# Kernel optimization log

Hardware: AMD Instinct MI355X
Metric: run time of the kernel (lower is better)

## Reference

```python
import jax, jax.numpy as jnp
import numpy as np

SCALES = (1, 2, 4, 8, 16, 32, 64, 128)
BETA = 0.25   # args.commit_beta
B, C, T = 64, 512, 128
Q, V = 8, 1024
DEPTH, K = 2, 3


def setup_inputs() -> dict:
    key = jax.random.key(0)
    k1, k2, k3, k4 = jax.random.split(key, 4)
    z = jax.random.normal(k1, (B, C, T), dtype=jnp.float32)
    codebooks = jax.random.normal(k2, (Q, V, C), dtype=jnp.float32)
    # small init so stacked ReLU convs stay numerically sane (fan_in = C*K)
    phi_w = jax.random.normal(k3, (Q, DEPTH, C, C, K), dtype=jnp.float32) * (1.0 / np.sqrt(C * K))
    phi_b = jax.random.normal(k4, (Q, DEPTH, C), dtype=jnp.float32) * 0.01
    return {"z": z, "codebooks": codebooks, "phi_w": phi_w, "phi_b": phi_b}


def _conv1d(x, w, b):
    # x: (B,C,T), w: (C_out,C_in,K), 'same' padding (K//2)
    y = jax.lax.conv_general_dilated(x, w, window_strides=(1,), padding=[(K // 2, K // 2)],
                                     dimension_numbers=('NCH', 'OIH', 'NCH'))
    return y + b[None, :, None]


def _phi(x, w_q, b_q):
    # Phi: DEPTH x (Conv1d + ReLU)
    for d in range(DEPTH):
        x = jax.nn.relu(_conv1d(x, w_q[d], b_q[d]))
    return x


def _quantize(xd, cb):
    # xd: (B,C,s) -> nearest codebook entry per timestep. cb: (V,C)
    s = xd.shape[-1]
    flat = xd.transpose(0, 2, 1).reshape(-1, C)                      # (B*s, C)
    d = (jnp.sum(flat * flat, axis=1, keepdims=True)
         - 2.0 * flat @ cb.T + jnp.sum(cb * cb, axis=1))            # (B*s, V)
    idx = jnp.argmin(d, axis=1)                                      # (B*s,)
    emb = cb[idx].reshape(B, s, C).transpose(0, 2, 1)                # (B,C,s)
    # straight-through (EMA codebook: no grad to codebook)
    quant = xd + jax.lax.stop_gradient(emb - xd)
    return quant, idx.reshape(B, s)


def reference(z, codebooks, phi_w, phi_b):
    z = z.astype(jnp.float32)
    z_ng = jax.lax.stop_gradient(z)
    z_q = z_ng
    z_hat = jnp.zeros_like(z_q)
    losses, usages, perps, all_idx = [], [], [], []
    for q, s in enumerate(SCALES):
        # area downsample == window mean (T divisible by s)
        xd = z_q.reshape(B, C, s, T // s).mean(axis=-1)              # (B,C,s)
        quant, idx = _quantize(xd, codebooks[q])
        up = quant if s == T else jax.image.resize(quant, (B, C, T), method='linear')
        z_hat_q = _phi(up, phi_w[q], phi_b[q])
        z_hat = z_hat + z_hat_q
        z_q = z_q - z_hat_q
        counts = jnp.zeros((V,), jnp.float32).at[idx.ravel()].add(1.0)
        usages.append(jnp.mean((counts > 0).astype(jnp.float32)) * 100.0)
        p = counts / (B * s)
        perps.append(jnp.exp(-jnp.sum(p * jnp.log(p + 1e-10))))
        losses.append(BETA * jnp.mean((jax.lax.stop_gradient(z_hat) - z) ** 2)
                      + jnp.mean((z_hat - z_ng) ** 2))
        all_idx.append(idx)
    nQ = float(len(SCALES))
    usage = sum(usages) / nQ
    loss = sum(losses) / nQ
    perp = sum(perps) / nQ
    z_hat_out = jax.lax.stop_gradient(z_hat) - z_ng + z              # straight-through output
    indices = jnp.concatenate([i for i in all_idx], axis=1)          # (B, sum(scales))
    return z_hat_out, usage, loss, perp, indices
```

## Files before the change

### kernel.cpp

```cpp
#include <hip/hip_runtime.h>
#include <math.h>

#define NB 64
#define NC 512
#define NT 128
#define NQ 8
#define NV 1024
#define NBIG 4194304
#define IDX_STRIDE 255

typedef _Float16 half_t;
typedef half_t f16x8 __attribute__((ext_vector_type(8)));
typedef float  f32x4 __attribute__((ext_vector_type(4)));

#define SC_MAIN 0.015625f
#define SC_MID  2.44140625e-4f

#define GLD16(g, l) __builtin_amdgcn_global_load_lds( \
    (const __attribute__((address_space(1))) unsigned int*)(g), \
    (__attribute__((address_space(3))) unsigned int*)(l), 16, 0, 0)

__device__ inline void split64(float v, half_t& h1, half_t& h2) {
    half_t a = (half_t)(v * 64.f);
    float r = v * 64.f - (float)a;
    h1 = a;
    h2 = (half_t)(r * 64.f);
}
__device__ inline void split1(float v, half_t& h1, half_t& h2) {
    half_t a = (half_t)v;
    float r = v - (float)a;
    h1 = a;
    h2 = (half_t)(r * 64.f);
}

__global__ void init_kernel(float* __restrict__ zhat, int* __restrict__ counts,
                            float* __restrict__ accums) {
    int i = blockIdx.x * 256 + threadIdx.x;
    const int stride = 2048 * 256;
    for (; i < NBIG; i += stride) {
        zhat[i] = 0.f;
        if (i < NQ * NV) counts[i] = 0;
        if (i < 16)      accums[i] = 0.f;
    }
}

__global__ void padzero_kernel(half_t* __restrict__ X1, half_t* __restrict__ X2) {
    int b = blockIdx.x;
    int row = blockIdx.y ? 129 : 0;
    int c = threadIdx.x;
    size_t off = ((size_t)b * 130 + row) * NC + c;
    X1[off] = (half_t)0.f; X2[off] = (half_t)0.f;
}

__global__ void cnorm_kernel(const float* __restrict__ cb, float* __restrict__ cnorm) {
    int wid  = (blockIdx.x * 256 + threadIdx.x) >> 6;
    int lane = threadIdx.x & 63;
    if (wid >= NQ * NV) return;
    const float* row = cb + (size_t)wid * NC;
    float s = 0.f;
    #pragma unroll
    for (int e = 0; e < NC / 64; ++e) { float v = row[lane + e * 64]; s = fmaf(v, v, s); }
    #pragma unroll
    for (int m = 32; m >= 1; m >>= 1) s += __shfl_xor(s, m, 64);
    if (lane == 0) cnorm[wid] = s;
}

__global__ void cbprep_kernel(const float* __restrict__ cb, half_t* __restrict__ CbT) {
    int idx = blockIdx.x * 256 + threadIdx.x;
    int e  = idx & 8191;
    int kt = (idx >> 13) & 7;
    int mt = (idx >> 16) & 7;
    int q  = idx >> 19;
    int m = e >> 6, kk = e & 63;
    int ci = kt * 64 + kk;
    int code = mt * 128 + m;
    float v = cb[((size_t)(q * NV + code)) * NC + ci];
    half_t h1, h2;
    split64(v, h1, h2);
    int off = ((m * 128 + kk * 2) ^ ((m & 7) << 4)) >> 1;
    size_t base = ((((size_t)q * 2 + 0) * 8 + mt) * 8 + kt) * 8192 + off;
    CbT[base] = h1;
    CbT[base + (size_t)8 * 8 * 8192] = h2;
}

__global__ __launch_bounds__(256) void downsample_split_kernel(
        const float* __restrict__ z, const float* __restrict__ zhat,
        half_t* __restrict__ Xd1, half_t* __restrict__ Xd2,
        int s, int log2s) {
    __shared__ float D[64 * 129];
    const int tid = threadIdx.x;
    const int b  = blockIdx.x;
    const int c0 = blockIdx.y << 6;
    const size_t gbase = ((size_t)(b * NC + c0)) * NT;
    #pragma unroll
    for (int i = 0; i < 8; ++i) {
        int idx4 = (i * 256 + tid) * 4;
        float4 zv = *(const float4*)(z    + gbase + idx4);
        float4 hv = *(const float4*)(zhat + gbase + idx4);
        int cc = idx4 >> 7, t = idx4 & 127;
        float* dp = D + cc * 129 + t;
        dp[0] = zv.x - hv.x; dp[1] = zv.y - hv.y; dp[2] = zv.z - hv.z; dp[3] = zv.w - hv.w;
    }
    __syncthreads();
    const int w = NT >> log2s;
    const float invw = 1.f / (float)w;
    for (int idx = tid; idx < (s << 6); idx += 256) {
        int cc = idx & 63;
        int j  = idx >> 6;
        const float* row = D + cc * 129 + j * w;
        float sum = 0.f;
        for (int i = 0; i < w; ++i) sum += row[i];
        float xd = sum * invw;
        half_t h1, h2;
        split1(xd, h1, h2);
        size_t o = ((size_t)(b * s + j)) * NC + c0 + cc;
        Xd1[o] = h1;
        Xd2[o] = h2;
    }
}

__global__ __launch_bounds__(256, 2) void quant_mfma_kernel(
        const half_t* __restrict__ CbTq,
        const half_t* __restrict__ Xd1, const half_t* __restrict__ Xd2,
        const float* __restrict__ cnorm,
        float* __restrict__ pval, int* __restrict__ pidx) {
    __shared__ half_t As1[8192];
    __shared__ half_t As2[8192];
    __shared__ half_t Bs1[4096];
    __shared__ half_t Bs2[4096];
    __shared__ float redv[2][2][2][16];
    __shared__ int   redi[2][2][2][16];
    const int tid = threadIdx.x;
    const int w = tid >> 6, l = tid & 63;
    const int wm = w >> 1, wn = w & 1;
    const int lane16 = l & 15, lhi = l >> 4;
    const int nblk = blockIdx.x, mt = blockIdx.y;
    const int r0 = nblk * 64;
    f32x4 accM[4][2] = {}, accm[4][2] = {};
    const half_t* C1b = CbTq + ((size_t)(0 * 8 + mt)) * (8 * 8192);
    const half_t* C2b = CbTq + ((size_t)(1 * 8 + mt)) * (8 * 8192);
    for (int kt = 0; kt < 8; ++kt) {
        const int ci0 = kt << 6;
        __syncthreads();
        const char* c1src = (const char*)(C1b + (size_t)kt * 8192);
        const char* c2src = (const char*)(C2b + (size_t)kt * 8192);
        #pragma unroll
        for (int i = 0; i < 4; ++i) {
            GLD16(c1src + (i * 256 + tid) * 16, (char*)As1 + i * 4096 + w * 1024);
            GLD16(c2src + (i * 256 + tid) * 16, (char*)As2 + i * 4096 + w * 1024);
        }
        #pragma unroll
        for (int i = 0; i < 2; ++i) {
            int c = i * 256 + tid;
            int n = c >> 3, sub = c & 7;
            size_t soff = ((size_t)(r0 + n)) * NC + ci0 + ((sub ^ (n & 7)) << 3);
            GLD16(Xd1 + soff, (char*)Bs1 + i * 4096 + w * 1024);
            GLD16(Xd2 + soff, (char*)Bs2 + i * 4096 + w * 1024);
        }
        __syncthreads();
        #pragma unroll
        for (int kstep = 0; kstep < 2; ++kstep) {
            const int kb = (kstep * 32 + lhi * 8) * 2;
            f16x8 a1[4], a2[4], b1[2], b2[2];
            #pragma unroll
            for (int im = 0; im < 4; ++im) {
                int m = wm * 64 + im * 16 + lane16;
                int off = (m * 128 + kb) ^ ((m & 7) << 4);
                a1[im] = *(const f16x8*)((const char*)As1 + off);
                a2[im] = *(const f16x8*)((const char*)As2 + off);
            }
            #pragma unroll
            for (int in = 0; in < 2; ++in) {
                int n = wn * 32 + in * 16 + lane16;
                int off = (n * 128 + kb) ^ ((n & 7) << 4);
                b1[in] = *(const f16x8*)((const char*)Bs1 + off);
                b2[in] = *(const f16x8*)((const char*)Bs2 + off);
            }
            #pragma unroll
            for (int im = 0; im < 4; ++im)
                #pragma unroll
                for (int in = 0; in < 2; ++in) {
                    accM[im][in] = __builtin_amdgcn_mfma_f32_16x16x32_f16(a1[im], b1[in], accM[im][in], 0, 0, 0);
                    accm[im][in] = __builtin_amdgcn_mfma_f32_16x16x32_f16(a1[im], b2[in], accm[im][in], 0, 0, 0);
                    accm[im][in] = __builtin_amdgcn_mfma_f32_16x16x32_f16(a2[im], b1[in], accm[im][in], 0, 0, 0);
                }
        }
    }
    float bv[2] = {1e30f, 1e30f};
    int   bi[2] = {0, 0};
    #pragma unroll
    for (int im = 0; im < 4; ++im) {
        int mb = mt * 128 + wm * 64 + im * 16 + lhi * 4;
        float4 cn = *(const float4*)(cnorm + mb);
        const float* cnp = (const float*)&cn;
        #pragma unroll
        for (int in = 0; in < 2; ++in) {
            #pragma unroll
            for (int r = 0; r < 4; ++r) {
                float d = cnp[r] - 2.f * (accM[im][in][r] * SC_MAIN + accm[im][in][r] * SC_MID);
                int code = mb + r;
                if (d < bv[in]) { bv[in] = d; bi[in] = code; }
            }
        }
    }
    #pragma unroll
    for (int m = 16; m <= 32; m <<= 1) {
        #pragma unroll
        for (int in = 0; in < 2; ++in) {
            float ov = __shfl_xor(bv[in], m, 64);
            int   oi = __shfl_xor(bi[in], m, 64);
            if (ov < bv[in] || (ov == bv[in] && oi < bi[in])) { bv[in] = ov; bi[in] = oi; }
        }
    }
    if (lhi == 0) {
        #pragma unroll
        for (int in = 0; in < 2; ++in) { redv[wm][wn][in][lane16] = bv[in]; redi[wm][wn][in][lane16] = bi[in]; }
    }
    __syncthreads();
    if (wm == 0 && lhi == 0) {
        #pragma unroll
        for (int in = 0; in < 2; ++in) {
            float v0 = redv[0][wn][in][lane16]; int i0 = redi[0][wn][in][lane16];
            float v1 = redv[1][wn][in][lane16]; int i1 = redi[1][wn][in][lane16];
            if (v1 < v0 || (v1 == v0 && i1 < i0)) { v0 = v1; i0 = i1; }
            int r = r0 + wn * 32 + in * 16 + lane16;
            pval[(size_t)r * 8 + mt] = v0;
            pidx[(size_t)r * 8 + mt] = i0;
        }
    }
}

__global__ void argmin_final_kernel(const float* __restrict__ pval, const int* __restrict__ pidx,
                                    int* __restrict__ idx_int, int* __restrict__ counts,
                                    float* __restrict__ out_idx, int R, int s, int log2s, int offq) {
    int r = blockIdx.x * 256 + threadIdx.x;
    if (r >= R) return;
    float bv = 1e30f; int bi = 0;
    #pragma unroll
    for (int k = 0; k < 8; ++k) {
        float v = pval[(size_t)r * 8 + k];
        int   i = pidx[(size_t)r * 8 + k];
        if (v < bv || (v == bv && i < bi)) { bv = v; bi = i; }
    }
    idx_int[r] = bi;
    atomicAdd(&counts[bi], 1);
    int b = r >> log2s, j = r & (s - 1);
    out_idx[(size_t)b * IDX_STRIDE + offq + j] = (float)bi;
}

__global__ void upsample_split_kernel(const float* __restrict__ cb, const int* __restrict__ idx_int,
                                      half_t* __restrict__ X1, half_t* __restrict__ X2, int s) {
    int b = blockIdx.x, tp = blockIdx.y, c = threadIdx.x;
    size_t off = ((size_t)b * 130 + tp) * NC + c;
    if (tp == 0 || tp == 129) { X1[off] = (half_t)0.f; X2[off] = (half_t)0.f; return; }
    int t = tp - 1;
    float in = (t + 0.5f) * ((float)s * (1.f / 128.f)) - 0.5f;
    float jf = floorf(in);
    float f = in - jf;
    int j0 = (int)jf;
    int i0 = min(max(j0, 0), s - 1);
    int i1 = min(max(j0 + 1, 0), s - 1);
    const int* ib = idx_int + b * s;
    float v0 = cb[(size_t)ib[i0] * NC + c];
    float v1 = cb[(size_t)ib[i1] * NC + c];
    float v = (1.f - f) * v0 + f * v1;
    half_t h1, h2;
    split1(v, h1, h2);
    X1[off] = h1; X2[off] = h2;
}

__global__ void wprep_kernel(const float* __restrict__ W ,
                             half_t* __restrict__ Wt) {
    int d = blockIdx.y;
    const float* Wd = W + (size_t)d * NC * NC * 3;
    half_t* Wtd = Wt + (size_t)d * (2 * 4 * 24 * 8192);
    int idx = blockIdx.x * 256 + threadIdx.x;
    int e  = idx & 8191;
    int rest = idx >> 13;
    int kt = rest % 24;
    int mtl = rest / 24;
    int m = e >> 6, kk = e & 63;
    int k = kt * 64 + kk;
    int ks = k >> 9, ci = k & 511;
    int co = mtl * 128 + m;
    float v = Wd[((size_t)co * NC + ci) * 3 + ks];
    half_t h1, h2;
    split64(v, h1, h2);
    int off = ((m * 128 + kk * 2) ^ ((m & 7) << 4)) >> 1;
    size_t base = ((size_t)mtl * 24 + kt) * 8192 + off;
    Wtd[base] = h1;
    Wtd[base + (size_t)4 * 24 * 8192] = h2;
}

template<int MODE>
__global__ __launch_bounds__(512) void conv_mfma_kernel(
        const half_t* __restrict__ Wt,
        const half_t* __restrict__ X1, const half_t* __restrict__ X2,
        const float* __restrict__ bias,
        half_t* __restrict__ Y1, half_t* __restrict__ Y2,
        float* __restrict__ zhat, const float* __restrict__ z,
        float* __restrict__ lpart) {
    __shared__ __align__(16) half_t A1a[8192], A2a[8192], B1a[8192], B2a[8192];
    __shared__ __align__(16) half_t A1b[8192], A2b[8192], B1b[8192], B2b[8192];
    const int tid = threadIdx.x;
    const int w = tid >> 6;
    const int wk = w >> 2;
    const int wm = (w >> 1) & 1, wn = w & 1;
    const int p  = w & 3;
    const int l = tid & 63, lane16 = l & 15, lhi = l >> 4;
    const int b = blockIdx.x, mt = blockIdx.y;
    f32x4 accM[4][4] = {}, accm[4][4] = {};
    const half_t* W1b = Wt + ((size_t)(0 * 4 + mt)) * (24 * 8192);
    const half_t* W2b = Wt + ((size_t)(1 * 4 + mt)) * (24 * 8192);

    auto stage = [&](half_t* dA1, half_t* dA2, half_t* dB1, half_t* dB2, int kt) {
        const int ks = kt >> 3, ci0 = (kt & 7) << 6;
        const char* s1 = (const char*)(W1b + (size_t)kt * 8192);
        const char* s2 = (const char*)(W2b + (size_t)kt * 8192);
        const int rowb0 = b * 130 + ks;
        #pragma unroll
        for (int i = 0; i < 2; ++i) {
            int doff = i * 8192 + w * 1024;
            GLD16(s1 + (i * 512 + tid) * 16, (char*)dA1 + doff);
            GLD16(s2 + (i * 512 + tid) * 16, (char*)dA2 + doff);
            int c = i * 512 + tid, n = c >> 3, sub = c & 7;
            size_t soff = (size_t)(rowb0 + n) * NC + ci0 + ((sub ^ (n & 7)) << 3);
            GLD16(X1 + soff, (char*)dB1 + doff);
            GLD16(X2 + soff, (char*)dB2 + doff);
        }
    };
    auto compute = [&](const half_t* A1, const half_t* A2, const half_t* B1, const half_t* B2) {
        const int kb = wk * 64 + lhi * 16;
        f16x8 a1[4], a2[4], b1[4], b2[4];
        #pragma unroll
        for (int im = 0; im < 4; ++im) {
            int m = wm * 64 + im * 16 + lane16;
            int off = (m * 128 + kb) ^ ((m & 7) << 4);
            a1[im] = *(const f16x8*)((const char*)A1 + off);
            a2[im] = *(const f16x8*)((const char*)A2 + off);
        }
        #pragma unroll
        for (int in = 0; in < 4; ++in) {
            int n = wn * 64 + in * 16 + lane16;
            int off = (n * 128 + kb) ^ ((n & 7) << 4);
            b1[in] = *(const f16x8*)((const char*)B1 + off);
            b2[in] = *(const f16x8*)((const char*)B2 + off);
        }
        __builtin_amdgcn_s_setprio(1);
        #pragma unroll
        for (int im = 0; im < 4; ++im)
            #pragma unroll
            for (int in = 0; in < 4; ++in) {
                accM[im][in] = __builtin_amdgcn_mfma_f32_16x16x32_f16(a1[im], b1[in], accM[im][in], 0, 0, 0);
                accm[im][in] = __builtin_amdgcn_mfma_f32_16x16x32_f16(a1[im], b2[in], accm[im][in], 0, 0, 0);
                accm[im][in] = __builtin_amdgcn_mfma_f32_16x16x32_f16(a2[im], b1[in], accm[im][in], 0, 0, 0);
            }
        __builtin_amdgcn_s_setprio(0);
    };

    stage(A1a, A2a, B1a, B2a, 0);
    __syncthreads();
    #pragma unroll 1
    for (int k2 = 0; k2 < 12; ++k2) {
        stage(A1b, A2b, B1b, B2b, 2 * k2 + 1);
        compute(A1a, A2a, B1a, B2a);
        __syncthreads();
        if (k2 < 11) stage(A1a, A2a, B1a, B2a, 2 * k2 + 2);
        compute(A1b, A2b, B1b, B2b);
        __syncthreads();
    }

    f32x4 y[4][4];
    #pragma unroll
    for (int im = 0; im < 4; ++im)
        #pragma unroll
        for (int in = 0; in < 4; ++in)
            #pragma unroll
            for (int r = 0; r < 4; ++r)
                y[im][in][r] = accM[im][in][r] * SC_MAIN + accm[im][in][r] * SC_MID;

    auto store_part = [&](f32x4* arr, int im) {
        #pragma unroll
        for (int in = 0; in < 4; ++in) arr[in * 256 + p * 64 + l] = y[im][in];
    };
    auto load_part = [&](const f32x4* arr, int im) {
        #pragma unroll
        for (int in = 0; in < 4; ++in) {
            f32x4 t = arr[in * 256 + p * 64 + l];
            #pragma unroll
            for (int r = 0; r < 4; ++r) y[im][in][r] += t[r];
        }
    };
    if (wk == 1) {
        store_part((f32x4*)A1b, 0); store_part((f32x4*)A2b, 1);
        store_part((f32x4*)B1b, 2); store_part((f32x4*)B2b, 3);
    }
    __syncthreads();

    float lsum = 0.f;
    if (wk == 0) {
        load_part((const f32x4*)A1b, 0); load_part((const f32x4*)A2b, 1);
        load_part((const f32x4*)B1b, 2); load_part((const f32x4*)B2b, 3);
        #pragma unroll
        for (int im = 0; im < 4; ++im) {
            int mb = mt * 128 + wm * 64 + im * 16 + lhi * 4;
            float bs[4];
            #pragma unroll
            for (int r = 0; r < 4; ++r) bs[r] = bias[mb + r];
            #pragma unroll
            for (int in = 0; in < 4; ++in) {
                int t = wn * 64 + in * 16 + lane16;
                if (MODE == 0) {
                    half_t h1v[4], h2v[4];
                    #pragma unroll
                    for (int r = 0; r < 4; ++r) {
                        float yy = y[im][in][r] + bs[r];
                        yy = yy > 0.f ? yy : 0.f;
                        split1(yy, h1v[r], h2v[r]);
                    }
                    size_t rowoff = ((size_t)(b * 130 + 1 + t)) * NC + mb;
                    *(ushort4*)(Y1 + rowoff) = *(const ushort4*)h1v;
                    *(ushort4*)(Y2 + rowoff) = *(const ushort4*)h2v;
                } else {
                    size_t base = ((size_t)b * NC + mb) * NT + t;
                    #pragma unroll
                    for (int r = 0; r < 4; ++r) {
                        float yy = y[im][in][r] + bs[r];
                        yy = yy > 0.f ? yy : 0.f;
                        size_t oi = base + (size_t)r * NT;
                        float zn = zhat[oi] + yy;
                        zhat[oi] = zn;
                        float d = zn - z[oi];
                        lsum = fmaf(d, d, lsum);
                    }
                }
            }
        }
    }
    if (MODE == 1) {
        __syncthreads();
        float* red = (float*)A1a;
        red[tid] = lsum;
        __syncthreads();
        for (int st = 256; st >= 1; st >>= 1) {
            if (tid < st) red[tid] += red[tid + st];
            __syncthreads();
        }
        if (tid == 0) lpart[blockIdx.y * 64 + blockIdx.x] = red[0];
    }
}

__global__ void scale_final_kernel(const float* __restrict__ lpart, const int* __restrict__ counts,
                                   float* __restrict__ accums, float invBS) {
    __shared__ float sm[256];
    __shared__ float se[256];
    __shared__ int   su[256];
    int tid = threadIdx.x;
    float ls = lpart[tid];
    int used = 0; float ent = 0.f;
    #pragma unroll
    for (int k = 0; k < 4; ++k) {
        int cv = counts[tid + k * 256];
        if (cv > 0) used++;
        float p = (float)cv * invBS;
        ent = fmaf(p, logf(p + 1e-10f), ent);
    }
    sm[tid] = ls; se[tid] = ent; su[tid] = used;
    __syncthreads();
    for (int st = 128; st >= 1; st >>= 1) {
        if (tid < st) { sm[tid] += sm[tid + st]; se[tid] += se[tid + st]; su[tid] += su[tid + st]; }
        __syncthreads();
    }
    if (tid == 0) {
        float m = sm[0] * (1.f / (float)NBIG);
        accums[1] += 0.25f * m + m;
        accums[0] += ((float)su[0] * (1.f / 1024.f)) * 100.f;
        accums[2] += expf(-se[0]);
    }
}

__global__ void final_write_kernel(const float* __restrict__ accums, float* __restrict__ outscal) {
    int t = threadIdx.x;
    if (t < 3) outscal[t] = accums[t] * 0.125f;
}

extern "C" void kernel_launch(void* const* d_in, const int* in_sizes, int n_in,
                              void* d_out, int out_size, void* d_ws, size_t ws_size,
                              hipStream_t stream) {
    const float* z  = (const float*)d_in[0];
    const float* cb = (const float*)d_in[1];
    const float* pw = (const float*)d_in[2];
    const float* pb = (const float*)d_in[3];

    float* zhat     = (float*)d_out;
    float* out_scal = zhat + NBIG;
    float* out_idx  = zhat + NBIG + 3;

    char* w = (char*)d_ws;
    half_t* Xd1 = (half_t*)w;  w += (size_t)8192 * NC * 2;
    half_t* Xd2 = (half_t*)w;  w += (size_t)8192 * NC * 2;
    half_t* Xa1 = (half_t*)w;  w += (size_t)NB * 130 * NC * 2;
    half_t* Xa2 = (half_t*)w;  w += (size_t)NB * 130 * NC * 2;
    half_t* Xb1 = (half_t*)w;  w += (size_t)NB * 130 * NC * 2;
    half_t* Xb2 = (half_t*)w;  w += (size_t)NB * 130 * NC * 2;
    half_t* Wt  = (half_t*)w;  w += (size_t)2 * 2 * 4 * 24 * 8192 * 2;
    half_t* CbT = (half_t*)w;  w += (size_t)NQ * 2 * 8 * 8 * 8192 * 2;
    float* pval  = (float*)w;  w += (size_t)8192 * 8 * 4;
    int*   pidx  = (int*)w;    w += (size_t)8192 * 8 * 4;
    int*   idx_i = (int*)w;    w += (size_t)16384 * 4;
    int*   counts= (int*)w;    w += (size_t)NQ * NV * 4;
    float* cnorm = (float*)w;  w += (size_t)NQ * NV * 4;
    float* lpart = (float*)w;  w += (size_t)256 * 4;
    float* accums= (float*)w;  w += 256;

    init_kernel<<<2048, 256, 0, stream>>>(zhat, counts, accums);
    padzero_kernel<<<dim3(64, 2), 512, 0, stream>>>(Xb1, Xb2);
    cnorm_kernel<<<(NQ * NV) / 4, 256, 0, stream>>>(cb, cnorm);
    cbprep_kernel<<<16384, 256, 0, stream>>>(cb, CbT);

    const size_t WT_CONV = (size_t)2 * 4 * 24 * 8192;
    int offq = 0;
    for (int q = 0; q < NQ; ++q) {
        int s = 1 << q;
        int R = NB * s;
        const float* cbq = cb + (size_t)q * NV * NC;
        const float* wq  = pw + (size_t)q * 2 * NC * NC * 3;
        const float* bq0 = pb + (size_t)q * 2 * NC;
        const float* bq1 = bq0 + NC;

        downsample_split_kernel<<<dim3(64, 8), 256, 0, stream>>>(z, zhat, Xd1, Xd2, s, q);
        quant_mfma_kernel<<<dim3(R / 64, 8), 256, 0, stream>>>(
            CbT + (size_t)q * 2 * 8 * 8 * 8192, Xd1, Xd2, cnorm + q * NV, pval, pidx);
        argmin_final_kernel<<<(R + 255) / 256, 256, 0, stream>>>(pval, pidx, idx_i,
                                                                 counts + q * NV, out_idx, R, s, q, offq);
        upsample_split_kernel<<<dim3(64, 130), 512, 0, stream>>>(cbq, idx_i, Xa1, Xa2, s);
        wprep_kernel<<<dim3(3072, 2), 256, 0, stream>>>(wq, Wt);
        conv_mfma_kernel<0><<<dim3(64, 4), 512, 0, stream>>>(
            Wt, Xa1, Xa2, bq0, Xb1, Xb2, nullptr, nullptr, nullptr);
        conv_mfma_kernel<1><<<dim3(64, 4), 512, 0, stream>>>(
            Wt + WT_CONV, Xb1, Xb2, bq1, nullptr, nullptr, zhat, z, lpart);
        scale_final_kernel<<<1, 256, 0, stream>>>(lpart, counts + q * NV, accums, 1.f / (float)(NB * s));
        offq += s;
    }
    final_write_kernel<<<1, 64, 0, stream>>>(accums, out_scal);
}
```

Measured before the change: 985.5 us.

## Interleave LDS loads, global staging and MFMA quarters in conv kernel; batch final reductions

The conv MFMA main loop is restructured so that each k-tile is processed in four quadrant steps. Each step loads a few LDS fragments, issues a slice of the next tile's global-to-LDS copies, and runs a quarter of the MFMAs, with s_barrier between steps. This interleaving is meant to overlap memory traffic with matrix work instead of staging a whole tile up front. Separately, the per-scale scalar reduction kernels and the final write are merged into one kernel launched once after the loop, with per-scale loss partials kept in a larger buffer, which drops the accumulator init and eight small launches. The extra barriers per tile could add stalls.

```diff
diff --git a/kernel.cpp b/kernel.cpp
--- a/kernel.cpp
+++ b/kernel.cpp
@@ -33,14 +33,12 @@
     h2 = (half_t)(r * 64.f);
 }
 
-__global__ void init_kernel(float* __restrict__ zhat, int* __restrict__ counts,
-                            float* __restrict__ accums) {
+__global__ void init_kernel(float* __restrict__ zhat, int* __restrict__ counts) {
     int i = blockIdx.x * 256 + threadIdx.x;
     const int stride = 2048 * 256;
     for (; i < NBIG; i += stride) {
         zhat[i] = 0.f;
         if (i < NQ * NV) counts[i] = 0;
-        if (i < 16)      accums[i] = 0.f;
     }
 }
 
@@ -312,61 +310,85 @@
     f32x4 accM[4][4] = {}, accm[4][4] = {};
     const half_t* W1b = Wt + ((size_t)(0 * 4 + mt)) * (24 * 8192);
     const half_t* W2b = Wt + ((size_t)(1 * 4 + mt)) * (24 * 8192);
-
-    auto stage = [&](half_t* dA1, half_t* dA2, half_t* dB1, half_t* dB2, int kt) {
-        const int ks = kt >> 3, ci0 = (kt & 7) << 6;
-        const char* s1 = (const char*)(W1b + (size_t)kt * 8192);
-        const char* s2 = (const char*)(W2b + (size_t)kt * 8192);
-        const int rowb0 = b * 130 + ks;
-        #pragma unroll
-        for (int i = 0; i < 2; ++i) {
-            int doff = i * 8192 + w * 1024;
-            GLD16(s1 + (i * 512 + tid) * 16, (char*)dA1 + doff);
-            GLD16(s2 + (i * 512 + tid) * 16, (char*)dA2 + doff);
-            int c = i * 512 + tid, n = c >> 3, sub = c & 7;
-            size_t soff = (size_t)(rowb0 + n) * NC + ci0 + ((sub ^ (n & 7)) << 3);
-            GLD16(X1 + soff, (char*)dB1 + doff);
-            GLD16(X2 + soff, (char*)dB2 + doff);
-        }
-    };
-    auto compute = [&](const half_t* A1, const half_t* A2, const half_t* B1, const half_t* B2) {
-        const int kb = wk * 64 + lhi * 16;
-        f16x8 a1[4], a2[4], b1[4], b2[4];
-        #pragma unroll
-        for (int im = 0; im < 4; ++im) {
-            int m = wm * 64 + im * 16 + lane16;
-            int off = (m * 128 + kb) ^ ((m & 7) << 4);
-            a1[im] = *(const f16x8*)((const char*)A1 + off);
-            a2[im] = *(const f16x8*)((const char*)A2 + off);
-        }
-        #pragma unroll
-        for (int in = 0; in < 4; ++in) {
-            int n = wn * 64 + in * 16 + lane16;
-            int off = (n * 128 + kb) ^ ((n & 7) << 4);
-            b1[in] = *(const f16x8*)((const char*)B1 + off);
-            b2[in] = *(const f16x8*)((const char*)B2 + off);
-        }
+    const int kb = wk * 64 + lhi * 16;
+
+    f16x8 a1[4], a2[4], b1[4], b2[4];
+
+    auto ldA = [&](const half_t* A1, const half_t* A2, int im) {
+        int m = wm * 64 + im * 16 + lane16;
+        int off = (m * 128 + kb) ^ ((m & 7) << 4);
+        a1[im] = *(const f16x8*)((const char*)A1 + off);
+        a2[im] = *(const f16x8*)((const char*)A2 + off);
+    };
+    auto ldB = [&](const half_t* B1, const half_t* B2, int in) {
+        int n = wn * 64 + in * 16 + lane16;
+        int off = (n * 128 + kb) ^ ((n & 7) << 4);
+        b1[in] = *(const f16x8*)((const char*)B1 + off);
+        b2[in] = *(const f16x8*)((const char*)B2 + off);
+    };
+    auto mmaq = [&](int im0, int in0) {
         __builtin_amdgcn_s_setprio(1);
         #pragma unroll
-        for (int im = 0; im < 4; ++im)
-            #pragma unroll
-            for (int in = 0; in < 4; ++in) {
+        for (int im = im0; im < im0 + 2; ++im)
+            #pragma unroll
+            for (int in = in0; in < in0 + 2; ++in) {
                 accM[im][in] = __builtin_amdgcn_mfma_f32_16x16x32_f16(a1[im], b1[in], accM[im][in], 0, 0, 0);
                 accm[im][in] = __builtin_amdgcn_mfma_f32_16x16x32_f16(a1[im], b2[in], accm[im][in], 0, 0, 0);
                 accm[im][in] = __builtin_amdgcn_mfma_f32_16x16x32_f16(a2[im], b1[in], accm[im][in], 0, 0, 0);
             }
         __builtin_amdgcn_s_setprio(0);
     };
-
-    stage(A1a, A2a, B1a, B2a, 0);
+    auto stage2 = [&](half_t* dA1, half_t* dA2, half_t* dB1, half_t* dB2, int kt, int pp) {
+        const int ks = kt >> 3, ci0 = (kt & 7) << 6;
+        #pragma unroll
+        for (int j = 0; j < 2; ++j) {
+            int c = 2 * pp + j;
+            int i = c >> 2, which = c & 3;
+            int doff = i * 8192 + w * 1024;
+            if (which == 0) {
+                GLD16((const char*)(W1b + (size_t)kt * 8192) + (i * 512 + tid) * 16, (char*)dA1 + doff);
+            } else if (which == 1) {
+                GLD16((const char*)(W2b + (size_t)kt * 8192) + (i * 512 + tid) * 16, (char*)dA2 + doff);
+            } else {
+                int cc = i * 512 + tid, n = cc >> 3, sub = cc & 7;
+                size_t soff = (size_t)(b * 130 + ks + n) * NC + ci0 + ((sub ^ (n & 7)) << 3);
+                if (which == 2) GLD16(X1 + soff, (char*)dB1 + doff);
+                else            GLD16(X2 + soff, (char*)dB2 + doff);
+            }
+        }
+    };
+    auto ktbody = [&](const half_t* CA1, const half_t* CA2, const half_t* CB1, const half_t* CB2,
+                      half_t* NA1, half_t* NA2, half_t* NB1, half_t* NB2, int ktn, bool doStage) {
+        ldA(CA1, CA2, 0); ldA(CA1, CA2, 1);
+        ldB(CB1, CB2, 0); ldB(CB1, CB2, 1);
+        if (doStage) stage2(NA1, NA2, NB1, NB2, ktn, 0);
+        __builtin_amdgcn_s_barrier();
+        mmaq(0, 0);
+        __builtin_amdgcn_s_barrier();
+        ldB(CB1, CB2, 2); ldB(CB1, CB2, 3);
+        if (doStage) stage2(NA1, NA2, NB1, NB2, ktn, 1);
+        __builtin_amdgcn_s_barrier();
+        mmaq(0, 2);
+        __builtin_amdgcn_s_barrier();
+        ldA(CA1, CA2, 2); ldA(CA1, CA2, 3);
+        if (doStage) stage2(NA1, NA2, NB1, NB2, ktn, 2);
+        __builtin_amdgcn_s_barrier();
+        mmaq(2, 2);
+        __builtin_amdgcn_s_barrier();
+        if (doStage) stage2(NA1, NA2, NB1, NB2, ktn, 3);
+        __builtin_amdgcn_s_barrier();
+        mmaq(2, 0);
+        __builtin_amdgcn_s_barrier();
+    };
+
+    stage2(A1a, A2a, B1a, B2a, 0, 0); stage2(A1a, A2a, B1a, B2a, 0, 1);
+    stage2(A1a, A2a, B1a, B2a, 0, 2); stage2(A1a, A2a, B1a, B2a, 0, 3);
     __syncthreads();
     #pragma unroll 1
     for (int k2 = 0; k2 < 12; ++k2) {
-        stage(A1b, A2b, B1b, B2b, 2 * k2 + 1);
-        compute(A1a, A2a, B1a, B2a);
-        __syncthreads();
-        if (k2 < 11) stage(A1a, A2a, B1a, B2a, 2 * k2 + 2);
-        compute(A1b, A2b, B1b, B2b);
+        ktbody(A1a, A2a, B1a, B2a, A1b, A2b, B1b, B2b, 2 * k2 + 1, true);
+        __syncthreads();
+        ktbody(A1b, A2b, B1b, B2b, A1a, A2a, B1a, B2a, 2 * k2 + 2, k2 < 11);
         __syncthreads();
     }
 
@@ -450,38 +472,43 @@
     }
 }
 
-__global__ void scale_final_kernel(const float* __restrict__ lpart, const int* __restrict__ counts,
-                                   float* __restrict__ accums, float invBS) {
+__global__ void scale_final_all_kernel(const float* __restrict__ lpart, const int* __restrict__ counts,
+                                       float* __restrict__ outscal) {
     __shared__ float sm[256];
     __shared__ float se[256];
     __shared__ int   su[256];
     int tid = threadIdx.x;
-    float ls = lpart[tid];
-    int used = 0; float ent = 0.f;
-    #pragma unroll
-    for (int k = 0; k < 4; ++k) {
-        int cv = counts[tid + k * 256];
-        if (cv > 0) used++;
-        float p = (float)cv * invBS;
-        ent = fmaf(p, logf(p + 1e-10f), ent);
-    }
-    sm[tid] = ls; se[tid] = ent; su[tid] = used;
-    __syncthreads();
-    for (int st = 128; st >= 1; st >>= 1) {
-        if (tid < st) { sm[tid] += sm[tid + st]; se[tid] += se[tid + st]; su[tid] += su[tid + st]; }
+    float aU = 0.f, aL = 0.f, aP = 0.f;
+    for (int q = 0; q < NQ; ++q) {
+        float invBS = 1.f / (float)(NB << q);
+        float ls = lpart[q * 256 + tid];
+        int used = 0; float ent = 0.f;
+        #pragma unroll
+        for (int k = 0; k < 4; ++k) {
+            int cv = counts[q * NV + tid + k * 256];
+            if (cv > 0) used++;
+            float pp = (float)cv * invBS;
+            ent = fmaf(pp, logf(pp + 1e-10f), ent);
+        }
+        sm[tid] = ls; se[tid] = ent; su[tid] = used;
+        __syncthreads();
+        for (int st = 128; st >= 1; st >>= 1) {
+            if (tid < st) { sm[tid] += sm[tid + st]; se[tid] += se[tid + st]; su[tid] += su[tid + st]; }
+            __syncthreads();
+        }
+        if (tid == 0) {
+            float m = sm[0] * (1.f / (float)NBIG);
+            aL += 0.25f * m + m;
+            aU += ((float)su[0] * (1.f / 1024.f)) * 100.f;
+            aP += expf(-se[0]);
+        }
         __syncthreads();
     }
     if (tid == 0) {
-        float m = sm[0] * (1.f / (float)NBIG);
-        accums[1] += 0.25f * m + m;
-        accums[0] += ((float)su[0] * (1.f / 1024.f)) * 100.f;
-        accums[2] += expf(-se[0]);
-    }
-}
-
-__global__ void final_write_kernel(const float* __restrict__ accums, float* __restrict__ outscal) {
-    int t = threadIdx.x;
-    if (t < 3) outscal[t] = accums[t] * 0.125f;
+        outscal[0] = aU * 0.125f;
+        outscal[1] = aL * 0.125f;
+        outscal[2] = aP * 0.125f;
+    }
 }
 
 extern "C" void kernel_launch(void* const* d_in, const int* in_sizes, int n_in,
@@ -510,10 +537,10 @@
     int*   idx_i = (int*)w;    w += (size_t)16384 * 4;
     int*   counts= (int*)w;    w += (size_t)NQ * NV * 4;
     float* cnorm = (float*)w;  w += (size_t)NQ * NV * 4;
-    float* lpart = (float*)w;  w += (size_t)256 * 4;
+    float* lpart = (float*)w;  w += (size_t)NQ * 256 * 4;
     float* accums= (float*)w;  w += 256;
 
-    init_kernel<<<2048, 256, 0, stream>>>(zhat, counts, accums);
+    init_kernel<<<2048, 256, 0, stream>>>(zhat, counts);
     padzero_kernel<<<dim3(64, 2), 512, 0, stream>>>(Xb1, Xb2);
     cnorm_kernel<<<(NQ * NV) / 4, 256, 0, stream>>>(cb, cnorm);
     cbprep_kernel<<<16384, 256, 0, stream>>>(cb, CbT);
@@ -538,9 +565,8 @@
         conv_mfma_kernel<0><<<dim3(64, 4), 512, 0, stream>>>(
             Wt, Xa1, Xa2, bq0, Xb1, Xb2, nullptr, nullptr, nullptr);
         conv_mfma_kernel<1><<<dim3(64, 4), 512, 0, stream>>>(
-            Wt + WT_CONV, Xb1, Xb2, bq1, nullptr, nullptr, zhat, z, lpart);
-        scale_final_kernel<<<1, 256, 0, stream>>>(lpart, counts + q * NV, accums, 1.f / (float)(NB * s));
+            Wt + WT_CONV, Xb1, Xb2, bq1, nullptr, nullptr, zhat, z, lpart + q * 256);
         offq += s;
     }
-    final_write_kernel<<<1, 64, 0, stream>>>(accums, out_scal);
-}
+    scale_final_all_kernel<<<1, 256, 0, stream>>>(lpart, counts, out_scal);
+}
```

Result: slower. 1.026 ms (+4.1%).

## Load conv B operand directly to registers; skip zhat zero-init and merge scalar reductions

Applied to the files above, without the earlier changes.

The conv kernel no longer stages the activation (B) tiles through LDS. Each wave now loads its B fragments straight from global memory into registers with double-buffering, which halves LDS use and removes the B ds_reads. The zhat zero-fill is dropped: the first scale reads only z in downsample and writes zhat directly in its second conv. The eight per-scale scalar-reduction launches and the final write are folded into one kernel at the end. The direct global B loads are uncoalesced 16-byte reads across rows and may raise memory latency in exchange for the lower LDS pressure and occupancy.

```diff
diff --git a/kernel.cpp b/kernel.cpp
--- a/kernel.cpp
+++ b/kernel.cpp
@@ -33,15 +33,9 @@
     h2 = (half_t)(r * 64.f);
 }
 
-__global__ void init_kernel(float* __restrict__ zhat, int* __restrict__ counts,
-                            float* __restrict__ accums) {
+__global__ void init_kernel(int* __restrict__ counts) {
     int i = blockIdx.x * 256 + threadIdx.x;
-    const int stride = 2048 * 256;
-    for (; i < NBIG; i += stride) {
-        zhat[i] = 0.f;
-        if (i < NQ * NV) counts[i] = 0;
-        if (i < 16)      accums[i] = 0.f;
-    }
+    if (i < NQ * NV) counts[i] = 0;
 }
 
 __global__ void padzero_kernel(half_t* __restrict__ X1, half_t* __restrict__ X2) {
@@ -86,20 +80,31 @@
 __global__ __launch_bounds__(256) void downsample_split_kernel(
         const float* __restrict__ z, const float* __restrict__ zhat,
         half_t* __restrict__ Xd1, half_t* __restrict__ Xd2,
-        int s, int log2s) {
+        int s, int log2s, int rdz) {
     __shared__ float D[64 * 129];
     const int tid = threadIdx.x;
     const int b  = blockIdx.x;
     const int c0 = blockIdx.y << 6;
     const size_t gbase = ((size_t)(b * NC + c0)) * NT;
-    #pragma unroll
-    for (int i = 0; i < 8; ++i) {
-        int idx4 = (i * 256 + tid) * 4;
-        float4 zv = *(const float4*)(z    + gbase + idx4);
-        float4 hv = *(const float4*)(zhat + gbase + idx4);
-        int cc = idx4 >> 7, t = idx4 & 127;
-        float* dp = D + cc * 129 + t;
-        dp[0] = zv.x - hv.x; dp[1] = zv.y - hv.y; dp[2] = zv.z - hv.z; dp[3] = zv.w - hv.w;
+    if (rdz) {
+        #pragma unroll
+        for (int i = 0; i < 8; ++i) {
+            int idx4 = (i * 256 + tid) * 4;
+            float4 zv = *(const float4*)(z    + gbase + idx4);
+            float4 hv = *(const float4*)(zhat + gbase + idx4);
+            int cc = idx4 >> 7, t = idx4 & 127;
+            float* dp = D + cc * 129 + t;
+            dp[0] = zv.x - hv.x; dp[1] = zv.y - hv.y; dp[2] = zv.z - hv.z; dp[3] = zv.w - hv.w;
+        }
+    } else {
+        #pragma unroll
+        for (int i = 0; i < 8; ++i) {
+            int idx4 = (i * 256 + tid) * 4;
+            float4 zv = *(const float4*)(z + gbase + idx4);
+            int cc = idx4 >> 7, t = idx4 & 127;
+            float* dp = D + cc * 129 + t;
+            dp[0] = zv.x; dp[1] = zv.y; dp[2] = zv.z; dp[3] = zv.w;
+        }
     }
     __syncthreads();
     const int w = NT >> log2s;
@@ -292,7 +297,7 @@
     Wtd[base + (size_t)4 * 24 * 8192] = h2;
 }
 
-template<int MODE>
+template<int MODE, int FIRST>
 __global__ __launch_bounds__(512) void conv_mfma_kernel(
         const half_t* __restrict__ Wt,
         const half_t* __restrict__ X1, const half_t* __restrict__ X2,
@@ -300,8 +305,8 @@
         half_t* __restrict__ Y1, half_t* __restrict__ Y2,
         float* __restrict__ zhat, const float* __restrict__ z,
         float* __restrict__ lpart) {
-    __shared__ __align__(16) half_t A1a[8192], A2a[8192], B1a[8192], B2a[8192];
-    __shared__ __align__(16) half_t A1b[8192], A2b[8192], B1b[8192], B2b[8192];
+    __shared__ __align__(16) half_t A1a[8192], A2a[8192];
+    __shared__ __align__(16) half_t A1b[8192], A2b[8192];
     const int tid = threadIdx.x;
     const int w = tid >> 6;
     const int wk = w >> 2;
@@ -312,39 +317,38 @@
     f32x4 accM[4][4] = {}, accm[4][4] = {};
     const half_t* W1b = Wt + ((size_t)(0 * 4 + mt)) * (24 * 8192);
     const half_t* W2b = Wt + ((size_t)(1 * 4 + mt)) * (24 * 8192);
-
-    auto stage = [&](half_t* dA1, half_t* dA2, half_t* dB1, half_t* dB2, int kt) {
-        const int ks = kt >> 3, ci0 = (kt & 7) << 6;
+    const int kbB = wk * 64 + lhi * 16;
+    const int cibase = wk * 32 + lhi * 8;
+
+    auto stageA = [&](half_t* dA1, half_t* dA2, int kt) {
         const char* s1 = (const char*)(W1b + (size_t)kt * 8192);
         const char* s2 = (const char*)(W2b + (size_t)kt * 8192);
-        const int rowb0 = b * 130 + ks;
         #pragma unroll
         for (int i = 0; i < 2; ++i) {
             int doff = i * 8192 + w * 1024;
             GLD16(s1 + (i * 512 + tid) * 16, (char*)dA1 + doff);
             GLD16(s2 + (i * 512 + tid) * 16, (char*)dA2 + doff);
-            int c = i * 512 + tid, n = c >> 3, sub = c & 7;
-            size_t soff = (size_t)(rowb0 + n) * NC + ci0 + ((sub ^ (n & 7)) << 3);
-            GLD16(X1 + soff, (char*)dB1 + doff);
-            GLD16(X2 + soff, (char*)dB2 + doff);
         }
     };
-    auto compute = [&](const half_t* A1, const half_t* A2, const half_t* B1, const half_t* B2) {
-        const int kb = wk * 64 + lhi * 16;
-        f16x8 a1[4], a2[4], b1[4], b2[4];
+    auto ldB = [&](f16x8* d1, f16x8* d2, int kt) {
+        const int ks = kt >> 3;
+        const int ci = ((kt & 7) << 6) + cibase;
+        #pragma unroll
+        for (int in = 0; in < 4; ++in) {
+            int n = wn * 64 + in * 16 + lane16;
+            size_t off = (size_t)(b * 130 + ks + n) * NC + ci;
+            d1[in] = *(const f16x8*)(X1 + off);
+            d2[in] = *(const f16x8*)(X2 + off);
+        }
+    };
+    auto compute = [&](const half_t* A1, const half_t* A2, const f16x8* b1, const f16x8* b2) {
+        f16x8 a1[4], a2[4];
         #pragma unroll
         for (int im = 0; im < 4; ++im) {
             int m = wm * 64 + im * 16 + lane16;
-            int off = (m * 128 + kb) ^ ((m & 7) << 4);
+            int off = (m * 128 + kbB) ^ ((m & 7) << 4);
             a1[im] = *(const f16x8*)((const char*)A1 + off);
             a2[im] = *(const f16x8*)((const char*)A2 + off);
-        }
-        #pragma unroll
-        for (int in = 0; in < 4; ++in) {
-            int n = wn * 64 + in * 16 + lane16;
-            int off = (n * 128 + kb) ^ ((n & 7) << 4);
-            b1[in] = *(const f16x8*)((const char*)B1 + off);
-            b2[in] = *(const f16x8*)((const char*)B2 + off);
         }
         __builtin_amdgcn_s_setprio(1);
         #pragma unroll
@@ -358,15 +362,18 @@
         __builtin_amdgcn_s_setprio(0);
     };
 
-    stage(A1a, A2a, B1a, B2a, 0);
+    f16x8 b1c[4], b2c[4], b1n[4], b2n[4];
+    stageA(A1a, A2a, 0);
+    ldB(b1c, b2c, 0);
     __syncthreads();
     #pragma unroll 1
     for (int k2 = 0; k2 < 12; ++k2) {
-        stage(A1b, A2b, B1b, B2b, 2 * k2 + 1);
-        compute(A1a, A2a, B1a, B2a);
-        __syncthreads();
-        if (k2 < 11) stage(A1a, A2a, B1a, B2a, 2 * k2 + 2);
-        compute(A1b, A2b, B1b, B2b);
+        stageA(A1b, A2b, 2 * k2 + 1);
+        ldB(b1n, b2n, 2 * k2 + 1);
+        compute(A1a, A2a, b1c, b2c);
+        __syncthreads();
+        if (k2 < 11) { stageA(A1a, A2a, 2 * k2 + 2); ldB(b1c, b2c, 2 * k2 + 2); }
+        compute(A1b, A2b, b1n, b2n);
         __syncthreads();
     }
 
@@ -392,15 +399,15 @@
         }
     };
     if (wk == 1) {
-        store_part((f32x4*)A1b, 0); store_part((f32x4*)A2b, 1);
-        store_part((f32x4*)B1b, 2); store_part((f32x4*)B2b, 3);
+        store_part((f32x4*)A1a, 0); store_part((f32x4*)A2a, 1);
+        store_part((f32x4*)A1b, 2); store_part((f32x4*)A2b, 3);
     }
     __syncthreads();
 
     float lsum = 0.f;
     if (wk == 0) {
-        load_part((const f32x4*)A1b, 0); load_part((const f32x4*)A2b, 1);
-        load_part((const f32x4*)B1b, 2); load_part((const f32x4*)B2b, 3);
+        load_part((const f32x4*)A1a, 0); load_part((const f32x4*)A2a, 1);
+        load_part((const f32x4*)A1b, 2); load_part((const f32x4*)A2b, 3);
         #pragma unroll
         for (int im = 0; im < 4; ++im) {
             int mb = mt * 128 + wm * 64 + im * 16 + lhi * 4;
@@ -428,7 +435,7 @@
                         float yy = y[im][in][r] + bs[r];
                         yy = yy > 0.f ? yy : 0.f;
                         size_t oi = base + (size_t)r * NT;
-                        float zn = zhat[oi] + yy;
+                        float zn = FIRST ? yy : (zhat[oi] + yy);
                         zhat[oi] = zn;
                         float d = zn - z[oi];
                         lsum = fmaf(d, d, lsum);
@@ -450,38 +457,43 @@
     }
 }
 
-__global__ void scale_final_kernel(const float* __restrict__ lpart, const int* __restrict__ counts,
-                                   float* __restrict__ accums, float invBS) {
+__global__ void scale_final_all_kernel(const float* __restrict__ lpart, const int* __restrict__ counts,
+                                       float* __restrict__ outscal) {
     __shared__ float sm[256];
     __shared__ float se[256];
     __shared__ int   su[256];
     int tid = threadIdx.x;
-    float ls = lpart[tid];
-    int used = 0; float ent = 0.f;
-    #pragma unroll
-    for (int k = 0; k < 4; ++k) {
-        int cv = counts[tid + k * 256];
-        if (cv > 0) used++;
-        float p = (float)cv * invBS;
-        ent = fmaf(p, logf(p + 1e-10f), ent);
-    }
-    sm[tid] = ls; se[tid] = ent; su[tid] = used;
-    __syncthreads();
-    for (int st = 128; st >= 1; st >>= 1) {
-        if (tid < st) { sm[tid] += sm[tid + st]; se[tid] += se[tid + st]; su[tid] += su[tid + st]; }
+    float aU = 0.f, aL = 0.f, aP = 0.f;
+    for (int q = 0; q < NQ; ++q) {
+        float invBS = 1.f / (float)(NB << q);
+        float ls = lpart[q * 256 + tid];
+        int used = 0; float ent = 0.f;
+        #pragma unroll
+        for (int k = 0; k < 4; ++k) {
+            int cv = counts[q * NV + tid + k * 256];
+            if (cv > 0) used++;
+            float pp = (float)cv * invBS;
+            ent = fmaf(pp, logf(pp + 1e-10f), ent);
+        }
+        sm[tid] = ls; se[tid] = ent; su[tid] = used;
+        __syncthreads();
+        for (int st = 128; st >= 1; st >>= 1) {
+            if (tid < st) { sm[tid] += sm[tid + st]; se[tid] += se[tid + st]; su[tid] += su[tid + st]; }
+            __syncthreads();
+        }
+        if (tid == 0) {
+            float m = sm[0] * (1.f / (float)NBIG);
+            aL += 0.25f * m + m;
+            aU += ((float)su[0] * (1.f / 1024.f)) * 100.f;
+            aP += expf(-se[0]);
+        }
         __syncthreads();
     }
     if (tid == 0) {
-        float m = sm[0] * (1.f / (float)NBIG);
-        accums[1] += 0.25f * m + m;
-        accums[0] += ((float)su[0] * (1.f / 1024.f)) * 100.f;
-        accums[2] += expf(-se[0]);
-    }
-}
-
-__global__ void final_write_kernel(const float* __restrict__ accums, float* __restrict__ outscal) {
-    int t = threadIdx.x;
-    if (t < 3) outscal[t] = accums[t] * 0.125f;
+        outscal[0] = aU * 0.125f;
+        outscal[1] = aL * 0.125f;
+        outscal[2] = aP * 0.125f;
+    }
 }
 
 extern "C" void kernel_launch(void* const* d_in, const int* in_sizes, int n_in,
@@ -510,10 +522,9 @@
     int*   idx_i = (int*)w;    w += (size_t)16384 * 4;
     int*   counts= (int*)w;    w += (size_t)NQ * NV * 4;
     float* cnorm = (float*)w;  w += (size_t)NQ * NV * 4;
-    float* lpart = (float*)w;  w += (size_t)256 * 4;
-    float* accums= (float*)w;  w += 256;
-
-    init_kernel<<<2048, 256, 0, stream>>>(zhat, counts, accums);
+    float* lpart = (float*)w;  w += (size_t)NQ * 256 * 4;
+
+    init_kernel<<<32, 256, 0, stream>>>(counts);
     padzero_kernel<<<dim3(64, 2), 512, 0, stream>>>(Xb1, Xb2);
     cnorm_kernel<<<(NQ * NV) / 4, 256, 0, stream>>>(cb, cnorm);
     cbprep_kernel<<<16384, 256, 0, stream>>>(cb, CbT);
@@ -528,19 +539,22 @@
         const float* bq0 = pb + (size_t)q * 2 * NC;
         const float* bq1 = bq0 + NC;
 
-        downsample_split_kernel<<<dim3(64, 8), 256, 0, stream>>>(z, zhat, Xd1, Xd2, s, q);
+        downsample_split_kernel<<<dim3(64, 8), 256, 0, stream>>>(z, zhat, Xd1, Xd2, s, q, q > 0 ? 1 : 0);
         quant_mfma_kernel<<<dim3(R / 64, 8), 256, 0, stream>>>(
             CbT + (size_t)q * 2 * 8 * 8 * 8192, Xd1, Xd2, cnorm + q * NV, pval, pidx);
         argmin_final_kernel<<<(R + 255) / 256, 256, 0, stream>>>(pval, pidx, idx_i,
                                                                  counts + q * NV, out_idx, R, s, q, offq);
         upsample_split_kernel<<<dim3(64, 130), 512, 0, stream>>>(cbq, idx_i, Xa1, Xa2, s);
         wprep_kernel<<<dim3(3072, 2), 256, 0, stream>>>(wq, Wt);
-        conv_mfma_kernel<0><<<dim3(64, 4), 512, 0, stream>>>(
+        conv_mfma_kernel<0, 0><<<dim3(64, 4), 512, 0, stream>>>(
             Wt, Xa1, Xa2, bq0, Xb1, Xb2, nullptr, nullptr, nullptr);
-        conv_mfma_kernel<1><<<dim3(64, 4), 512, 0, stream>>>(
-            Wt + WT_CONV, Xb1, Xb2, bq1, nullptr, nullptr, zhat, z, lpart);
-        scale_final_kernel<<<1, 256, 0, stream>>>(lpart, counts + q * NV, accums, 1.f / (float)(NB * s));
+        if (q == 0)
+            conv_mfma_kernel<1, 1><<<dim3(64, 4), 512, 0, stream>>>(
+                Wt + WT_CONV, Xb1, Xb2, bq1, nullptr, nullptr, zhat, z, lpart + q * 256);
+        else
+            conv_mfma_kernel<1, 0><<<dim3(64, 4), 512, 0, stream>>>(
+                Wt + WT_CONV, Xb1, Xb2, bq1, nullptr, nullptr, zhat, z, lpart + q * 256);
         offq += s;
     }
-    final_write_kernel<<<1, 64, 0, stream>>>(accums, out_scal);
-}
+    scale_final_all_kernel<<<1, 256, 0, stream>>>(lpart, counts, out_scal);
+}
```

Measured after the change: 1.404 ms. 1.42x slower.
